# Performance work log

Hardware: AMD Instinct MI355X
Metric: run time of the kernel (lower is better)

The kernel has to match this reference:

```python
import jax, jax.numpy as jnp
import numpy as np

NUM_HEADS = 12
DIM = 768
HEAD_DIM = DIM // NUM_HEADS


def setup_inputs() -> dict:
    key = jax.random.key(0)
    k1, k2, k3, k4 = jax.random.split(key, 4)
    B, N, C = 4, 8192, DIM
    x = jax.random.normal(k1, (B, N, C), dtype=jnp.float32)
    # torch nn.Linear stores weight as (out_features, in_features)
    W_qkv = jax.random.normal(k2, (3 * C, C), dtype=jnp.float32) * (1.0 / np.sqrt(C))
    W_proj = jax.random.normal(k3, (C, C), dtype=jnp.float32) * (1.0 / np.sqrt(C))
    b_proj = jax.random.normal(k4, (C,), dtype=jnp.float32) * 0.01
    return {"x": x, "W_qkv": W_qkv, "W_proj": W_proj, "b_proj": b_proj}


def reference(x, W_qkv, W_proj, b_proj):
    B, N, C = x.shape
    H, D = NUM_HEADS, HEAD_DIM
    qkv = x @ W_qkv.T                                  # [B,N,3C]
    qkv = qkv.reshape(B, N, 3, H, D).transpose(2, 0, 3, 1, 4)  # [3,B,H,N,D]
    q, k, v = qkv[0], qkv[1], qkv[2]
    q = jax.nn.elu(q) + 1.0
    k = jax.nn.elu(k) + 1.0
    k_sum = k.sum(axis=-2)                             # [B,H,D]
    kv = jnp.einsum('bhnd,bhne->bhde', k, v)           # [B,H,D,D]
    numerator = jnp.einsum('bhnd,bhde->bhne', q, kv)   # [B,H,N,D]
    denominator = jnp.einsum('bhnd,bhd->bhn', q, k_sum)
    out = numerator / (denominator[..., None] + 1e-6)
    out = out.transpose(0, 2, 1, 3).reshape(B, N, C)   # [B,N,C]
    out = out @ W_proj.T + b_proj
    return out
```

## Files before the change

kernel.cpp:

```cpp
#include <hip/hip_runtime.h>
#include <hip/hip_bf16.h>
#include <stdint.h>

typedef __attribute__((ext_vector_type(8))) short short8;
typedef __attribute__((ext_vector_type(4))) float floatx4;

#define NB 4
#define NN 8192
#define NC 768
#define NH 12
#define ND 64
#define LDQKV 2304

__device__ __forceinline__ float bf2f(ushort u) {
    union { float f; uint32_t i; } x; x.i = ((uint32_t)u) << 16; return x.f;
}
__device__ __forceinline__ ushort f2bf(float f) {
    union { float f; uint32_t i; } x; x.f = f;
    uint32_t r = x.i + 0x7fff + ((x.i >> 16) & 1);
    return (ushort)(r >> 16);
}
typedef const __attribute__((address_space(1))) uint32_t* gas1_t;
typedef __attribute__((address_space(3))) uint32_t* las3_t;
__device__ __forceinline__ void gl_lds16(const void* g, const void* l) {
    __builtin_amdgcn_global_load_lds((gas1_t)(uintptr_t)g,
                                     (las3_t)(uint32_t)(uintptr_t)l, 16, 0, 0);
}

__global__ __launch_bounds__(256) void cvt_bf16(const float* __restrict__ src,
                                                ushort* __restrict__ dst, int n) {
    const int i = (blockIdx.x * 256 + threadIdx.x) * 8;
    if (i >= n) return;
    const float4 a = *(const float4*)(src + i);
    const float4 b = *(const float4*)(src + i + 4);
    short8 v;
    v[0] = (short)f2bf(a.x); v[1] = (short)f2bf(a.y);
    v[2] = (short)f2bf(a.z); v[3] = (short)f2bf(a.w);
    v[4] = (short)f2bf(b.x); v[5] = (short)f2bf(b.y);
    v[6] = (short)f2bf(b.z); v[7] = (short)f2bf(b.w);
    *(short8*)(dst + i) = v;
}

template<int LDC, bool ELU, bool BIAS, typename OutT>
__global__ __launch_bounds__(256) void gemm_bt(const ushort* __restrict__ A,
                                               const ushort* __restrict__ Bw,
                                               const float* __restrict__ bias,
                                               OutT* __restrict__ Cout, int K) {
    __shared__ ushort As[128 * 32];
    __shared__ ushort Bs[128 * 32];
    const int t = threadIdx.x;
    const int w = t >> 6, lane = t & 63, l16 = lane & 15, quad = lane >> 4;
    const int wm = w & 1, wn = w >> 1;
    const int m0 = blockIdx.y * 128, n0 = blockIdx.x * 128;

    floatx4 acc[4][4] = {};

    const int rowA = t >> 2, chA = t & 3;
    const ushort* gA = A  + (size_t)(m0 + rowA) * K + chA * 8;
    const ushort* gB = Bw + (size_t)(n0 + rowA) * K + chA * 8;

    for (int k0 = 0; k0 < K; k0 += 32) {
        gl_lds16(gA + k0,                As + w * 512);
        gl_lds16(gA + k0 + 64 * K,       As + 2048 + w * 512);
        gl_lds16(gB + k0,                Bs + w * 512);
        gl_lds16(gB + k0 + 64 * K,       Bs + 2048 + w * 512);
        __syncthreads();
        short8 af[4], bfr[4];
        #pragma unroll
        for (int i = 0; i < 4; i++)
            af[i] = *(const short8*)&As[(wm * 64 + i * 16 + l16) * 32 + quad * 8];
        #pragma unroll
        for (int j = 0; j < 4; j++)
            bfr[j] = *(const short8*)&Bs[(wn * 64 + j * 16 + l16) * 32 + quad * 8];
        #pragma unroll
        for (int i = 0; i < 4; i++)
            #pragma unroll
            for (int j = 0; j < 4; j++)
                acc[i][j] = __builtin_amdgcn_mfma_f32_16x16x32_bf16(af[i], bfr[j], acc[i][j], 0, 0, 0);
        __syncthreads();
    }

    #pragma unroll
    for (int i = 0; i < 4; i++) {
        const int row = m0 + wm * 64 + i * 16 + quad * 4;
        #pragma unroll
        for (int j = 0; j < 4; j++) {
            const int col = n0 + wn * 64 + j * 16 + l16;
            float bval = 0.f;
            if (BIAS) bval = bias[col];
            #pragma unroll
            for (int r = 0; r < 4; r++) {
                float v = acc[i][j][r];
                if (ELU) { if (col < 2 * NC) v = (v > 0.f) ? v + 1.f : __expf(v); }
                if (BIAS) v += bval;
                if (sizeof(OutT) == 2) Cout[(size_t)(row + r) * LDC + col] = (OutT)f2bf(v);
                else                   Cout[(size_t)(row + r) * LDC + col] = (OutT)v;
            }
        }
    }
}

__global__ __launch_bounds__(256) void kv_ksum(const ushort* __restrict__ qkv,
                                               float* __restrict__ kvws,
                                               float* __restrict__ ksws) {
    __shared__ ushort klds[128 * 64];
    __shared__ ushort vlds[128 * 64];
    __shared__ float  kvred[64 * 64];
    __shared__ float  ksred[4][64];
    const int bh = blockIdx.y, b = bh / NH, h = bh % NH;
    const int t = threadIdx.x, w = t >> 6, lane = t & 63, l16 = lane & 15, quad = lane >> 4;
    const int n0 = blockIdx.x * 1024;
    const ushort* kbase = qkv + (size_t)(b * NN) * LDQKV + NC     + h * ND;
    const ushort* vbase = qkv + (size_t)(b * NN) * LDQKV + 2 * NC + h * ND;

    floatx4 acc[4][4] = {};
    float ksp = 0.f;
    const int rowT = t >> 3, ch = t & 7;

    for (int s = 0; s < 8; s++) {
        const int nb = n0 + s * 128;
        #pragma unroll
        for (int i = 0; i < 4; i++) {
            const size_t r = (size_t)(nb + i * 32 + rowT) * LDQKV + ch * 8;
            gl_lds16(kbase + r, klds + i * 2048 + w * 512);
            gl_lds16(vbase + r, vlds + i * 2048 + w * 512);
        }
        __syncthreads();
        short8 af[4], bfr[4];
        #pragma unroll
        for (int dt = 0; dt < 4; dt++) {
            short8 v;
            #pragma unroll
            for (int j = 0; j < 8; j++)
                v[j] = (short)klds[(w * 32 + quad * 8 + j) * 64 + dt * 16 + l16];
            af[dt] = v;
        }
        #pragma unroll
        for (int et = 0; et < 4; et++) {
            short8 v;
            #pragma unroll
            for (int j = 0; j < 8; j++)
                v[j] = (short)vlds[(w * 32 + quad * 8 + j) * 64 + et * 16 + l16];
            bfr[et] = v;
        }
        #pragma unroll
        for (int dt = 0; dt < 4; dt++)
            #pragma unroll
            for (int et = 0; et < 4; et++)
                acc[dt][et] = __builtin_amdgcn_mfma_f32_16x16x32_bf16(af[dt], bfr[et], acc[dt][et], 0, 0, 0);
        #pragma unroll
        for (int n = 0; n < 32; n++) ksp += bf2f(klds[(w * 32 + n) * 64 + lane]);
        __syncthreads();
    }

    if (w == 0) {
        #pragma unroll
        for (int dt = 0; dt < 4; dt++)
            #pragma unroll
            for (int et = 0; et < 4; et++)
                #pragma unroll
                for (int r = 0; r < 4; r++)
                    kvred[(dt * 16 + quad * 4 + r) * 64 + et * 16 + l16] = acc[dt][et][r];
    }
    ksred[w][lane] = ksp;
    __syncthreads();
    if (w != 0) {
        #pragma unroll
        for (int dt = 0; dt < 4; dt++)
            #pragma unroll
            for (int et = 0; et < 4; et++)
                #pragma unroll
                for (int r = 0; r < 4; r++)
                    atomicAdd(&kvred[(dt * 16 + quad * 4 + r) * 64 + et * 16 + l16], acc[dt][et][r]);
    }
    __syncthreads();
    for (int i = t; i < 4096; i += 256) atomicAdd(&kvws[(size_t)bh * 4096 + i], kvred[i]);
    if (t < 64) atomicAdd(&ksws[bh * 64 + t], ksred[0][t] + ksred[1][t] + ksred[2][t] + ksred[3][t]);
}

__global__ __launch_bounds__(256) void attn_apply(const ushort* __restrict__ qkv,
                                                  const float* __restrict__ kvws,
                                                  const float* __restrict__ ksws,
                                                  ushort* __restrict__ outpre) {
    __shared__ ushort kvb[64 * 80];
    const int bh = blockIdx.y, b = bh / NH, h = bh % NH;
    const int t = threadIdx.x, w = t >> 6, lane = t & 63, l16 = lane & 15, quad = lane >> 4;

    for (int i = t; i < 4096; i += 256) {
        const int d = i >> 6, e = i & 63;
        kvb[d * 80 + e] = f2bf(kvws[(size_t)bh * 4096 + i]);
    }
    for (int i = t; i < 1024; i += 256) {
        const int d = i >> 4, c = i & 15;
        kvb[d * 80 + 64 + c] = (c == 0) ? f2bf(ksws[bh * 64 + d]) : (ushort)0;
    }
    __syncthreads();

    short8 bfr[5][2];
    #pragma unroll
    for (int et = 0; et < 5; et++)
        #pragma unroll
        for (int ks = 0; ks < 2; ks++) {
            short8 v;
            #pragma unroll
            for (int j = 0; j < 8; j++)
                v[j] = (short)kvb[(ks * 32 + quad * 8 + j) * 80 + et * 16 + l16];
            bfr[et][ks] = v;
        }

    const ushort* qbase = qkv + (size_t)(b * NN) * LDQKV + h * ND;
    ushort* obase = outpre + (size_t)(b * NN) * NC + h * ND;
    const int n0 = blockIdx.x * 1024;

    for (int it = 0; it < 16; it++) {
        const int nt = n0 + (it * 4 + w) * 16;
        const ushort* qp = qbase + (size_t)(nt + l16) * LDQKV + quad * 8;
        const short8 a0 = *(const short8*)qp;
        const short8 a1 = *(const short8*)(qp + 32);
        floatx4 acc[5] = {};
        #pragma unroll
        for (int et = 0; et < 5; et++) {
            acc[et] = __builtin_amdgcn_mfma_f32_16x16x32_bf16(a0, bfr[et][0], acc[et], 0, 0, 0);
            acc[et] = __builtin_amdgcn_mfma_f32_16x16x32_bf16(a1, bfr[et][1], acc[et], 0, 0, 0);
        }
        float dv[4];
        #pragma unroll
        for (int r = 0; r < 4; r++) dv[r] = __shfl(acc[4][r], lane & 48);
        #pragma unroll
        for (int et = 0; et < 4; et++)
            #pragma unroll
            for (int r = 0; r < 4; r++) {
                const float o = acc[et][r] / (dv[r] + 1e-6f);
                obase[(size_t)(nt + quad * 4 + r) * NC + et * 16 + l16] = f2bf(o);
            }
    }
}

__global__ void zero_f32(float* p, int n) {
    const int i = blockIdx.x * 256 + threadIdx.x;
    if (i < n) p[i] = 0.f;
}

extern "C" void kernel_launch(void* const* d_in, const int* in_sizes, int n_in,
                              void* d_out, int out_size, void* d_ws, size_t ws_size,
                              hipStream_t stream) {
    (void)in_sizes; (void)n_in; (void)out_size; (void)ws_size;
    const float* X     = (const float*)d_in[0];
    const float* Wqkv  = (const float*)d_in[1];
    const float* Wproj = (const float*)d_in[2];
    const float* bproj = (const float*)d_in[3];
    float* out = (float*)d_out;

    char* ws = (char*)d_ws;
    size_t off = 0;
    ushort* qkv     = (ushort*)(ws + off); off += (size_t)32768 * 2304 * 2;
    ushort* outpre  = (ushort*)(ws + off); off += (size_t)32768 * 768 * 2;
    ushort* xbf     = (ushort*)(ws + off); off += (size_t)32768 * 768 * 2;
    ushort* wqkvbf  = (ushort*)(ws + off); off += (size_t)2304 * 768 * 2;
    ushort* wprojbf = (ushort*)(ws + off); off += (size_t)768 * 768 * 2;
    float*  kvws    = (float*)(ws + off);  off += (size_t)48 * 4096 * 4;
    float*  ksws    = (float*)(ws + off);

    const int nx = 32768 * 768, nwq = 2304 * 768, nwp = 768 * 768;
    cvt_bf16<<<nx  / (256 * 8), 256, 0, stream>>>(X,     xbf,     nx);
    cvt_bf16<<<nwq / (256 * 8), 256, 0, stream>>>(Wqkv,  wqkvbf,  nwq);
    cvt_bf16<<<nwp / (256 * 8), 256, 0, stream>>>(Wproj, wprojbf, nwp);

    const int nzero = 48 * 4096 + 48 * 64;
    zero_f32<<<(nzero + 255) / 256, 256, 0, stream>>>(kvws, nzero);

    gemm_bt<LDQKV, true, false, ushort><<<dim3(18, 256), 256, 0, stream>>>(xbf, wqkvbf, nullptr, qkv, NC);
    kv_ksum<<<dim3(8, 48), 256, 0, stream>>>(qkv, kvws, ksws);
    attn_apply<<<dim3(8, 48), 256, 0, stream>>>(qkv, kvws, ksws, outpre);
    gemm_bt<NC, false, true, float><<<dim3(6, 256), 256, 0, stream>>>(outpre, wprojbf, bproj, out, NC);
}
```

Before: 490.3 us.

## Replace GEMM with 256x256 tile, 8-wave double-buffered pipelined kernel

Replaces the 128x128 single-buffer bf16 GEMM with a 256x256-tile kernel using 512 threads, double-buffered LDS with 64-wide K steps, XOR-swizzled LDS layout, and a four-phase schedule that interleaves global-to-LDS prefetches with MFMA blocks. It also remaps workgroup IDs for better cache locality and raises wave priority during MFMA phases. The goal is to hide global load latency, cut the barrier stall per K step, and raise operand reuse per LDS load. The cost is 128KB of LDS and many more registers per block, which lowers occupancy, and the projection GEMM launches only 384 blocks.

```diff
diff --git a/kernel.cpp b/kernel.cpp
--- a/kernel.cpp
+++ b/kernel.cpp
@@ -41,56 +41,156 @@
     *(short8*)(dst + i) = v;
 }
 
+
+__device__ __forceinline__ void stage_half(const ushort* __restrict__ src, int row0,
+                                           int k0, int K, ushort* dst, int t, int w) {
+    const int rsub = t >> 3;
+    const int ch = (t & 7) ^ (rsub & 7);
+    const ushort* g0 = src + (size_t)(row0 + rsub) * K + k0 + ch * 8;
+    gl_lds16(g0,                 dst + w * 512);
+    gl_lds16(g0 + (size_t)64 * K, dst + 4096 + w * 512);
+}
+
+#define PHASE_SYNC() do {                                        \
+    __builtin_amdgcn_s_barrier();                                \
+    asm volatile("s_waitcnt lgkmcnt(0)" ::: "memory");           \
+    __builtin_amdgcn_sched_barrier(0);                           \
+} while (0)
+
 template<int LDC, bool ELU, bool BIAS, typename OutT>
-__global__ __launch_bounds__(256) void gemm_bt(const ushort* __restrict__ A,
+__global__ __launch_bounds__(512) void gemm256(const ushort* __restrict__ A,
                                                const ushort* __restrict__ Bw,
                                                const float* __restrict__ bias,
                                                OutT* __restrict__ Cout, int K) {
-    __shared__ ushort As[128 * 32];
-    __shared__ ushort Bs[128 * 32];
-    const int t = threadIdx.x;
-    const int w = t >> 6, lane = t & 63, l16 = lane & 15, quad = lane >> 4;
-    const int wm = w & 1, wn = w >> 1;
-    const int m0 = blockIdx.y * 128, n0 = blockIdx.x * 128;
-
-    floatx4 acc[4][4] = {};
-
-    const int rowA = t >> 2, chA = t & 3;
-    const ushort* gA = A  + (size_t)(m0 + rowA) * K + chA * 8;
-    const ushort* gB = Bw + (size_t)(n0 + rowA) * K + chA * 8;
-
-    for (int k0 = 0; k0 < K; k0 += 32) {
-        gl_lds16(gA + k0,                As + w * 512);
-        gl_lds16(gA + k0 + 64 * K,       As + 2048 + w * 512);
-        gl_lds16(gB + k0,                Bs + w * 512);
-        gl_lds16(gB + k0 + 64 * K,       Bs + 2048 + w * 512);
-        __syncthreads();
-        short8 af[4], bfr[4];
-        #pragma unroll
-        for (int i = 0; i < 4; i++)
-            af[i] = *(const short8*)&As[(wm * 64 + i * 16 + l16) * 32 + quad * 8];
-        #pragma unroll
-        for (int j = 0; j < 4; j++)
-            bfr[j] = *(const short8*)&Bs[(wn * 64 + j * 16 + l16) * 32 + quad * 8];
-        #pragma unroll
-        for (int i = 0; i < 4; i++)
-            #pragma unroll
-            for (int j = 0; j < 4; j++)
-                acc[i][j] = __builtin_amdgcn_mfma_f32_16x16x32_bf16(af[i], bfr[j], acc[i][j], 0, 0, 0);
-        __syncthreads();
+    __shared__ __align__(16) ushort SL[2][4][8192];
+    const int t = threadIdx.x, w = t >> 6, lane = t & 63;
+    const int l16 = lane & 15, quad = lane >> 4;
+    const int wm = w >> 2, wn = w & 3;
+    const int bro = (wn & 1) * 64;
+
+    const int gx = gridDim.x;
+    const int nwg = gx * gridDim.y;
+    int bid = blockIdx.y * gx + blockIdx.x;
+    bid = (bid & 7) * (nwg >> 3) + (bid >> 3);
+    const int m0 = (bid / gx) * 256;
+    const int n0 = (bid % gx) * 256;
+    const int NT = K >> 6;
+
+    floatx4 acc[8][4] = {};
+    short8 af[4][2], b01[2][2], b23[2][2];
+
+    stage_half(Bw, n0,       0,  K, &SL[0][0][0], t, w);
+    stage_half(Bw, n0 + 128, 0,  K, &SL[0][1][0], t, w);
+    stage_half(A,  m0,       0,  K, &SL[0][2][0], t, w);
+    stage_half(A,  m0 + 128, 0,  K, &SL[0][3][0], t, w);
+    stage_half(Bw, n0,       64, K, &SL[1][0][0], t, w);
+    stage_half(Bw, n0 + 128, 64, K, &SL[1][1][0], t, w);
+    asm volatile("s_waitcnt vmcnt(4)" ::: "memory");
+    __builtin_amdgcn_s_barrier();
+
+    for (int j = 0; j < NT; j++) {
+        const int buf = j & 1;
+        const ushort* As = &SL[buf][2 + wm][0];
+        const ushort* Bs = &SL[buf][wn >> 1][0];
+
+        #pragma unroll
+        for (int mi = 0; mi < 4; mi++) {
+            const int row = mi * 16 + l16;
+            const int sw = (row & 7) << 3;
+            const int base = row * 64 + quad * 8;
+            af[mi][0] = *(const short8*)&As[base ^ sw];
+            af[mi][1] = *(const short8*)&As[(base + 32) ^ sw];
+        }
+        #pragma unroll
+        for (int ni = 0; ni < 2; ni++) {
+            const int row = bro + ni * 16 + l16;
+            const int sw = (row & 7) << 3;
+            const int base = row * 64 + quad * 8;
+            b01[ni][0] = *(const short8*)&Bs[base ^ sw];
+            b01[ni][1] = *(const short8*)&Bs[(base + 32) ^ sw];
+        }
+        if (j + 1 < NT) stage_half(A, m0, (j + 1) * 64, K, &SL[buf ^ 1][2][0], t, w);
+        PHASE_SYNC();
+        __builtin_amdgcn_s_setprio(1);
+        #pragma unroll
+        for (int mi = 0; mi < 4; mi++)
+            #pragma unroll
+            for (int ni = 0; ni < 2; ni++) {
+                acc[mi][ni] = __builtin_amdgcn_mfma_f32_16x16x32_bf16(af[mi][0], b01[ni][0], acc[mi][ni], 0, 0, 0);
+                acc[mi][ni] = __builtin_amdgcn_mfma_f32_16x16x32_bf16(af[mi][1], b01[ni][1], acc[mi][ni], 0, 0, 0);
+            }
+        __builtin_amdgcn_s_setprio(0);
+        __builtin_amdgcn_s_barrier();
+
+        #pragma unroll
+        for (int ni = 0; ni < 2; ni++) {
+            const int row = bro + (2 + ni) * 16 + l16;
+            const int sw = (row & 7) << 3;
+            const int base = row * 64 + quad * 8;
+            b23[ni][0] = *(const short8*)&Bs[base ^ sw];
+            b23[ni][1] = *(const short8*)&Bs[(base + 32) ^ sw];
+        }
+        if (j + 1 < NT) stage_half(A, m0 + 128, (j + 1) * 64, K, &SL[buf ^ 1][3][0], t, w);
+        PHASE_SYNC();
+        __builtin_amdgcn_s_setprio(1);
+        #pragma unroll
+        for (int mi = 0; mi < 4; mi++)
+            #pragma unroll
+            for (int ni = 0; ni < 2; ni++) {
+                acc[mi][2 + ni] = __builtin_amdgcn_mfma_f32_16x16x32_bf16(af[mi][0], b23[ni][0], acc[mi][2 + ni], 0, 0, 0);
+                acc[mi][2 + ni] = __builtin_amdgcn_mfma_f32_16x16x32_bf16(af[mi][1], b23[ni][1], acc[mi][2 + ni], 0, 0, 0);
+            }
+        __builtin_amdgcn_s_setprio(0);
+        __builtin_amdgcn_s_barrier();
+
+        #pragma unroll
+        for (int mi = 0; mi < 4; mi++) {
+            const int row = (4 + mi) * 16 + l16;
+            const int sw = (row & 7) << 3;
+            const int base = row * 64 + quad * 8;
+            af[mi][0] = *(const short8*)&As[base ^ sw];
+            af[mi][1] = *(const short8*)&As[(base + 32) ^ sw];
+        }
+        if (j + 2 < NT) stage_half(Bw, n0, (j + 2) * 64, K, &SL[buf][0][0], t, w);
+        PHASE_SYNC();
+        __builtin_amdgcn_s_setprio(1);
+        #pragma unroll
+        for (int mi = 0; mi < 4; mi++)
+            #pragma unroll
+            for (int ni = 0; ni < 2; ni++) {
+                acc[4 + mi][ni] = __builtin_amdgcn_mfma_f32_16x16x32_bf16(af[mi][0], b01[ni][0], acc[4 + mi][ni], 0, 0, 0);
+                acc[4 + mi][ni] = __builtin_amdgcn_mfma_f32_16x16x32_bf16(af[mi][1], b01[ni][1], acc[4 + mi][ni], 0, 0, 0);
+            }
+        __builtin_amdgcn_s_setprio(0);
+        __builtin_amdgcn_s_barrier();
+
+        if (j + 2 < NT) stage_half(Bw, n0 + 128, (j + 2) * 64, K, &SL[buf][1][0], t, w);
+        __builtin_amdgcn_s_barrier();
+        __builtin_amdgcn_s_setprio(1);
+        #pragma unroll
+        for (int mi = 0; mi < 4; mi++)
+            #pragma unroll
+            for (int ni = 0; ni < 2; ni++) {
+                acc[4 + mi][2 + ni] = __builtin_amdgcn_mfma_f32_16x16x32_bf16(af[mi][0], b23[ni][0], acc[4 + mi][2 + ni], 0, 0, 0);
+                acc[4 + mi][2 + ni] = __builtin_amdgcn_mfma_f32_16x16x32_bf16(af[mi][1], b23[ni][1], acc[4 + mi][2 + ni], 0, 0, 0);
+            }
+        __builtin_amdgcn_s_setprio(0);
+        if (j < NT - 2) asm volatile("s_waitcnt vmcnt(4)" ::: "memory");
+        else            asm volatile("s_waitcnt vmcnt(0)" ::: "memory");
+        __builtin_amdgcn_s_barrier();
     }
 
     #pragma unroll
-    for (int i = 0; i < 4; i++) {
-        const int row = m0 + wm * 64 + i * 16 + quad * 4;
-        #pragma unroll
-        for (int j = 0; j < 4; j++) {
-            const int col = n0 + wn * 64 + j * 16 + l16;
+    for (int mi = 0; mi < 8; mi++) {
+        const int row = m0 + wm * 128 + mi * 16 + quad * 4;
+        #pragma unroll
+        for (int n = 0; n < 4; n++) {
+            const int col = n0 + wn * 64 + n * 16 + l16;
             float bval = 0.f;
             if (BIAS) bval = bias[col];
             #pragma unroll
             for (int r = 0; r < 4; r++) {
-                float v = acc[i][j][r];
+                float v = acc[mi][n][r];
                 if (ELU) { if (col < 2 * NC) v = (v > 0.f) ? v + 1.f : __expf(v); }
                 if (BIAS) v += bval;
                 if (sizeof(OutT) == 2) Cout[(size_t)(row + r) * LDC + col] = (OutT)f2bf(v);
@@ -269,8 +369,8 @@
     const int nzero = 48 * 4096 + 48 * 64;
     zero_f32<<<(nzero + 255) / 256, 256, 0, stream>>>(kvws, nzero);
 
-    gemm_bt<LDQKV, true, false, ushort><<<dim3(18, 256), 256, 0, stream>>>(xbf, wqkvbf, nullptr, qkv, NC);
+    gemm256<LDQKV, true, false, ushort><<<dim3(9, 128), 512, 0, stream>>>(xbf, wqkvbf, nullptr, qkv, NC);
     kv_ksum<<<dim3(8, 48), 256, 0, stream>>>(qkv, kvws, ksws);
     attn_apply<<<dim3(8, 48), 256, 0, stream>>>(qkv, kvws, ksws, outpre);
-    gemm_bt<NC, false, true, float><<<dim3(6, 256), 256, 0, stream>>>(outpre, wprojbf, bproj, out, NC);
-}
+    gemm256<NC, false, true, float><<<dim3(3, 128), 512, 0, stream>>>(outpre, wprojbf, bproj, out, NC);
+}
```

Result: faster. 465.2 us (-5.1%).
